# Kernel optimization log

Hardware: AMD Instinct MI355X
Metric: run time of the kernel (lower is better)

Reference implementation:

```python
import jax, jax.numpy as jnp
import numpy as np

N_NODES = 100000


def gcn_conv(x, W, b, src, dst, norm, n):
    # x: [N, Fin] -> [N, Fout]; PyG GCNConv: linear, then normalized scatter-add
    h = x @ W                                   # [N, Fout]
    msgs = h[src] * norm[:, None]               # gather + degree-normalize, [E2, Fout]
    out = jax.ops.segment_sum(msgs, dst, num_segments=n)  # scatter-add
    return out + b


def _norm_and_loops(edge_index, n):
    # add self-loops and compute symmetric normalization deg^-1/2 * deg^-1/2
    src = jnp.concatenate([edge_index[0], jnp.arange(n)])
    dst = jnp.concatenate([edge_index[1], jnp.arange(n)])
    deg = jax.ops.segment_sum(jnp.ones_like(dst, dtype=jnp.float32), dst, num_segments=n)
    dinv = jnp.where(deg > 0, jax.lax.rsqrt(jnp.maximum(deg, 1.0)), 0.0)
    norm = dinv[src] * dinv[dst]
    return src, dst, norm


def setup_inputs() -> dict:
    key = jax.random.key(0)
    ks = jax.random.split(key, 10)
    F_IN, H, C = 128, 128, 40
    x = jax.random.normal(ks[0], (N_NODES, F_IN), dtype=jnp.float32)
    edge_index = jax.random.randint(ks[1], (2, 3200000), 0, N_NODES, dtype=jnp.int64)
    def glorot(k, fan_in, fan_out):
        s = jnp.sqrt(6.0 / (fan_in + fan_out))
        return jax.random.uniform(k, (fan_in, fan_out), jnp.float32, -s, s)
    return {
        'x': x,
        'edge_index': edge_index,
        'W1': glorot(ks[2], F_IN, H), 'b1': jnp.zeros((H,), jnp.float32),
        'W2': glorot(ks[3], H, H),    'b2': jnp.zeros((H,), jnp.float32),
        'W3': glorot(ks[4], H, H),    'b3': jnp.zeros((H,), jnp.float32),
        'Wc': glorot(ks[5], H, C),    'bc': jnp.zeros((C,), jnp.float32),
    }


def reference(x, edge_index, W1, b1, W2, b2, W3, b3, Wc, bc):
    n = x.shape[0]
    src, dst, norm = _norm_and_loops(edge_index, n)
    h = jnp.tanh(gcn_conv(x, W1, b1, src, dst, norm, n))
    h = jnp.tanh(gcn_conv(h, W2, b2, src, dst, norm, n))
    h = jnp.tanh(gcn_conv(h, W3, b3, src, dst, norm, n))
    out = h @ Wc + bc
    return (out, h)
```

## Files before the change

### kernel.cpp

```cpp
#include <hip/hip_runtime.h>
#include <hip/hip_fp16.h>
#include <math.h>

#define H 128
#define BSTRIDE 5120
#define NPH 25


__global__ __launch_bounds__(256) void bin_kernel(const int* __restrict__ src,
        const int* __restrict__ dst, int* __restrict__ bucketFill,
        int* __restrict__ packed, int E, int nbk) {
    __shared__ int hcnt[1024];
    __shared__ int base[1024];
    __shared__ int cur[1024];
    int tid = threadIdx.x;
    for (int i = tid; i < nbk; i += 256) { hcnt[i] = 0; cur[i] = 0; }
    __syncthreads();
    int e0 = blockIdx.x * 8192;
    int e1 = min(e0 + 8192, E);
    for (int e = e0 + tid; e < e1; e += 256)
        atomicAdd(&hcnt[dst[e] >> 7], 1);
    __syncthreads();
    for (int i = tid; i < nbk; i += 256) {
        int c = hcnt[i];
        base[i] = c ? atomicAdd(&bucketFill[i], c) : 0;
    }
    __syncthreads();
    for (int e = e0 + tid; e < e1; e += 256) {
        int d = dst[e], s = src[e];
        int b = d >> 7;
        int r = atomicAdd(&cur[b], 1);
        packed[b * BSTRIDE + base[b] + r] = ((d & 127) << 17) | s;
    }
}

__global__ __launch_bounds__(256) void fine_kernel(const int* __restrict__ packed,
        const int* __restrict__ bucketFill,
        int* __restrict__ rowptr, int* __restrict__ col, float* __restrict__ dinv,
        int N, int E) {
    __shared__ int cnt[128 * NPH];
    __shared__ int cur[128 * NPH];
    __shared__ int lcnt[128], lofs[128];
    __shared__ int red[256];
    int b = blockIdx.x;
    int tid = threadIdx.x;
    int m = bucketFill[b]; if (m > BSTRIDE) m = BSTRIDE;
    int n0 = b << 7;

    int psum = 0;
    for (int i = tid; i < b; i += 256) psum += bucketFill[i];
    red[tid] = psum;
    for (int i = tid; i < 128 * NPH; i += 256) cnt[i] = 0;
    __syncthreads();
    #pragma unroll
    for (int off = 128; off > 0; off >>= 1) {
        if (tid < off) red[tid] += red[tid + off];
        __syncthreads();
    }
    int base = red[0];
    if (b == 0 && tid == 0) rowptr[N] = E;

    const int* pk = packed + (size_t)b * BSTRIDE;
    for (int i = tid; i < m; i += 256) {
        int p = pk[i];
        int ld = p >> 17, s = p & 131071;
        atomicAdd(&cnt[ld * NPH + (s >> 12)], 1);
    }
    __syncthreads();
    if (tid < 128) {
        int t = 0;
        #pragma unroll
        for (int q = 0; q < NPH; ++q) t += cnt[tid * NPH + q];
        lcnt[tid] = t;
    }
    __syncthreads();
    if (tid == 0) {
        int acc = 0;
        #pragma unroll 4
        for (int i = 0; i < 128; ++i) { lofs[i] = acc; acc += lcnt[i]; }
    }
    __syncthreads();
    if (tid < 128) {
        int o = lofs[tid];
        #pragma unroll
        for (int q = 0; q < NPH; ++q) {
            int c = cnt[tid * NPH + q];
            cur[tid * NPH + q] = o;
            o += c;
        }
        int node = n0 + tid;
        if (node < N) {
            rowptr[node] = base + lofs[tid];
            dinv[node] = rsqrtf((float)(lcnt[tid] + 1));
        }
    }
    __syncthreads();
    for (int i = tid; i < m; i += 256) {
        int p = pk[i];
        int ld = p >> 17, s = p & 131071;
        int r = atomicAdd(&cur[ld * NPH + (s >> 12)], 1);
        col[base + r] = s;
    }
}


__device__ inline unsigned pack2(float x, float y) {
    __half2 h = __floats2half2_rn(x, y);
    return *(unsigned*)&h;
}

__global__ __launch_bounds__(256) void gemm128_kernel(const float* __restrict__ A,
        const float* __restrict__ W, const float* __restrict__ scale,
        unsigned short* __restrict__ C, int N) {
    __shared__ float As[64][H + 1];
    int tid = threadIdx.x;
    int r0 = blockIdx.x * 64;

    #pragma unroll
    for (int i = 0; i < 8; ++i) {
        int lin = tid + i * 256;
        int r = lin >> 5;
        int c4 = (lin & 31) << 2;
        float4 v = make_float4(0.f, 0.f, 0.f, 0.f);
        if (r0 + r < N) v = *(const float4*)&A[(size_t)(r0 + r) * H + c4];
        As[r][c4 + 0] = v.x; As[r][c4 + 1] = v.y;
        As[r][c4 + 2] = v.z; As[r][c4 + 3] = v.w;
    }
    __syncthreads();

    int row = tid & 63;
    int c0 = __builtin_amdgcn_readfirstlane((tid >> 6) << 5);

    float acc[32];
    #pragma unroll
    for (int j = 0; j < 32; ++j) acc[j] = 0.f;

    for (int k = 0; k < H; ++k) {
        float a = As[row][k];
        #pragma unroll
        for (int j = 0; j < 32; ++j)
            acc[j] = fmaf(a, W[k * H + c0 + j], acc[j]);
    }

    int gr = r0 + row;
    if (gr < N) {
        float s = scale[gr];
        unsigned short* Crow = C + (size_t)gr * H;
        #pragma unroll
        for (int j = 0; j < 32; j += 8) {
            uint4 w;
            w.x = pack2(acc[j + 0] * s, acc[j + 1] * s);
            w.y = pack2(acc[j + 2] * s, acc[j + 3] * s);
            w.z = pack2(acc[j + 4] * s, acc[j + 5] * s);
            w.w = pack2(acc[j + 6] * s, acc[j + 7] * s);
            *(uint4*)&Crow[c0 + j] = w;
        }
    }
}


__device__ inline void add8(float* a, uint4 v) {
    float2 f;
    f = __half22float2(*(const __half2*)&v.x); a[0] += f.x; a[1] += f.y;
    f = __half22float2(*(const __half2*)&v.y); a[2] += f.x; a[3] += f.y;
    f = __half22float2(*(const __half2*)&v.z); a[4] += f.x; a[5] += f.y;
    f = __half22float2(*(const __half2*)&v.w); a[6] += f.x; a[7] += f.y;
}

__global__ __launch_bounds__(256) void spmm_kernel(const unsigned short* __restrict__ lin,
        const int* __restrict__ rowptr, const int* __restrict__ col,
        const float* __restrict__ dinv, const float* __restrict__ bias,
        float* __restrict__ out, int N) {
    int tid = threadIdx.x;
    int node = blockIdx.x * 16 + (tid >> 4);
    if (node >= N) return;
    int cq = tid & 15;

    int beg = rowptr[node];
    int end = rowptr[node + 1];

    const uint4* linv = (const uint4*)lin;

    float acc[8];
    {
        uint4 sv = linv[(size_t)node * 16 + cq];
        float2 f;
        f = __half22float2(*(const __half2*)&sv.x); acc[0] = f.x; acc[1] = f.y;
        f = __half22float2(*(const __half2*)&sv.y); acc[2] = f.x; acc[3] = f.y;
        f = __half22float2(*(const __half2*)&sv.z); acc[4] = f.x; acc[5] = f.y;
        f = __half22float2(*(const __half2*)&sv.w); acc[6] = f.x; acc[7] = f.y;
    }

    int e = beg;
    for (; e + 4 <= end; e += 4) {
        int s0 = col[e], s1 = col[e + 1], s2 = col[e + 2], s3 = col[e + 3];
        uint4 v0 = linv[(size_t)s0 * 16 + cq];
        uint4 v1 = linv[(size_t)s1 * 16 + cq];
        uint4 v2 = linv[(size_t)s2 * 16 + cq];
        uint4 v3 = linv[(size_t)s3 * 16 + cq];
        add8(acc, v0);
        add8(acc, v1);
        add8(acc, v2);
        add8(acc, v3);
    }
    for (; e < end; ++e) {
        uint4 v = linv[(size_t)col[e] * 16 + cq];
        add8(acc, v);
    }

    float d = dinv[node];
    int c8 = cq << 3;
    float4 r0, r1;
    r0.x = tanhf(fmaf(acc[0], d, bias[c8 + 0]));
    r0.y = tanhf(fmaf(acc[1], d, bias[c8 + 1]));
    r0.z = tanhf(fmaf(acc[2], d, bias[c8 + 2]));
    r0.w = tanhf(fmaf(acc[3], d, bias[c8 + 3]));
    r1.x = tanhf(fmaf(acc[4], d, bias[c8 + 4]));
    r1.y = tanhf(fmaf(acc[5], d, bias[c8 + 5]));
    r1.z = tanhf(fmaf(acc[6], d, bias[c8 + 6]));
    r1.w = tanhf(fmaf(acc[7], d, bias[c8 + 7]));
    float4* op = (float4*)out + (size_t)node * 32 + (cq << 1);
    op[0] = r0;
    op[1] = r1;
}


__global__ __launch_bounds__(256) void classifier_kernel(const float* __restrict__ h,
        const float* __restrict__ Wc, const float* __restrict__ bc,
        float* __restrict__ out, int N, int Cout) {
    __shared__ float As[64][H + 1];
    int tid = threadIdx.x;
    int r0 = blockIdx.x * 64;

    #pragma unroll
    for (int i = 0; i < 8; ++i) {
        int lin = tid + i * 256;
        int r = lin >> 5;
        int c4 = (lin & 31) << 2;
        float4 v = make_float4(0.f, 0.f, 0.f, 0.f);
        if (r0 + r < N) v = *(const float4*)&h[(size_t)(r0 + r) * H + c4];
        As[r][c4 + 0] = v.x; As[r][c4 + 1] = v.y;
        As[r][c4 + 2] = v.z; As[r][c4 + 3] = v.w;
    }
    __syncthreads();

    int row = tid & 63;
    int c0 = __builtin_amdgcn_readfirstlane((tid >> 6) * 10);

    float acc[10];
    #pragma unroll
    for (int j = 0; j < 10; ++j) acc[j] = bc[c0 + j];

    for (int k = 0; k < H; ++k) {
        float a = As[row][k];
        #pragma unroll
        for (int j = 0; j < 10; ++j)
            acc[j] = fmaf(a, Wc[k * Cout + c0 + j], acc[j]);
    }

    int gr = r0 + row;
    if (gr < N) {
        float* orow = out + (size_t)gr * Cout + c0;
        #pragma unroll
        for (int j = 0; j < 10; ++j) orow[j] = acc[j];
    }
}


extern "C" void kernel_launch(void* const* d_in, const int* in_sizes, int n_in,
                              void* d_out, int out_size, void* d_ws, size_t ws_size,
                              hipStream_t stream) {
    const float* x  = (const float*)d_in[0];
    const int* eidx = (const int*)d_in[1];
    const float* W1 = (const float*)d_in[2];
    const float* b1 = (const float*)d_in[3];
    const float* W2 = (const float*)d_in[4];
    const float* b2 = (const float*)d_in[5];
    const float* W3 = (const float*)d_in[6];
    const float* b3 = (const float*)d_in[7];
    const float* Wc = (const float*)d_in[8];
    const float* bc = (const float*)d_in[9];

    int N    = in_sizes[0] / H;
    int E    = in_sizes[1] / 2;
    int Cout = in_sizes[8] / H;
    int nbk  = (N + 127) >> 7;

    const int* srcp = eidx;
    const int* dstp = eidx + E;

    float* out  = (float*)d_out;
    float* hOut = out + (size_t)N * Cout;

    char* p = (char*)d_ws;
    float* hAf      = (float*)p;  p += (size_t)N * H * 4;
    int*   col      = (int*)p;    p += (size_t)E * 4;
    int*   rowptr   = (int*)p;    p += (size_t)(N + 1) * 4;
    float* dinv     = (float*)p;  p += (size_t)N * 4;
    int*   bFill    = (int*)p;    p += 1024 * 4;
    unsigned short* hA = (unsigned short*)hAf;
    int*   packed   = (int*)hAf;

    int gg = (N + 63) / 64;
    int gs = (N + 15) / 16;
    int gb = (E + 8191) / 8192;

    hipMemsetAsync(bFill, 0, (size_t)nbk * 4, stream);
    bin_kernel<<<gb, 256, 0, stream>>>(srcp, dstp, bFill, packed, E, nbk);
    fine_kernel<<<nbk, 256, 0, stream>>>(packed, bFill, rowptr, col, dinv, N, E);

    gemm128_kernel<<<gg, 256, 0, stream>>>(x, W1, dinv, hA, N);
    spmm_kernel<<<gs, 256, 0, stream>>>(hA, rowptr, col, dinv, b1, hOut, N);
    gemm128_kernel<<<gg, 256, 0, stream>>>(hOut, W2, dinv, hA, N);
    spmm_kernel<<<gs, 256, 0, stream>>>(hA, rowptr, col, dinv, b2, hOut, N);
    gemm128_kernel<<<gg, 256, 0, stream>>>(hOut, W3, dinv, hA, N);
    spmm_kernel<<<gs, 256, 0, stream>>>(hA, rowptr, col, dinv, b3, hOut, N);
    classifier_kernel<<<gg, 256, 0, stream>>>(hOut, Wc, bc, out, N, Cout);
}
```

Before: 803.7 us.

## Use fp16 MFMA matrix cores for the dense 128x128 GEMM

Replaces the scalar FP32 FMA loop in the per-layer linear transform with MFMA 16x16x32 fp16 instructions. Inputs and the transposed weight are converted to fp16 and staged in padded shared memory. Each wave computes a 64x32 output tile. This removes the ALU-bound inner loop but lowers input precision to fp16, and the output stores become scattered 2-byte writes instead of 16-byte vector stores.

```diff
diff --git a/kernel.cpp b/kernel.cpp
--- a/kernel.cpp
+++ b/kernel.cpp
@@ -5,6 +5,9 @@
 #define H 128
 #define BSTRIDE 5120
 #define NPH 25
+
+typedef _Float16 f16x8 __attribute__((ext_vector_type(8)));
+typedef float f32x4 __attribute__((ext_vector_type(4)));
 
 
 __global__ __launch_bounds__(256) void bin_kernel(const int* __restrict__ src,
@@ -104,15 +107,11 @@
 }
 
 
-__device__ inline unsigned pack2(float x, float y) {
-    __half2 h = __floats2half2_rn(x, y);
-    return *(unsigned*)&h;
-}
-
 __global__ __launch_bounds__(256) void gemm128_kernel(const float* __restrict__ A,
         const float* __restrict__ W, const float* __restrict__ scale,
         unsigned short* __restrict__ C, int N) {
-    __shared__ float As[64][H + 1];
+    __shared__ _Float16 Ah[64][H + 8];
+    __shared__ _Float16 Wt[H][H + 8];
     int tid = threadIdx.x;
     int r0 = blockIdx.x * 64;
 
@@ -123,37 +122,63 @@
         int c4 = (lin & 31) << 2;
         float4 v = make_float4(0.f, 0.f, 0.f, 0.f);
         if (r0 + r < N) v = *(const float4*)&A[(size_t)(r0 + r) * H + c4];
-        As[r][c4 + 0] = v.x; As[r][c4 + 1] = v.y;
-        As[r][c4 + 2] = v.z; As[r][c4 + 3] = v.w;
-    }
-    __syncthreads();
-
-    int row = tid & 63;
-    int c0 = __builtin_amdgcn_readfirstlane((tid >> 6) << 5);
-
-    float acc[32];
-    #pragma unroll
-    for (int j = 0; j < 32; ++j) acc[j] = 0.f;
-
-    for (int k = 0; k < H; ++k) {
-        float a = As[row][k];
-        #pragma unroll
-        for (int j = 0; j < 32; ++j)
-            acc[j] = fmaf(a, W[k * H + c0 + j], acc[j]);
-    }
-
-    int gr = r0 + row;
-    if (gr < N) {
-        float s = scale[gr];
-        unsigned short* Crow = C + (size_t)gr * H;
-        #pragma unroll
-        for (int j = 0; j < 32; j += 8) {
-            uint4 w;
-            w.x = pack2(acc[j + 0] * s, acc[j + 1] * s);
-            w.y = pack2(acc[j + 2] * s, acc[j + 3] * s);
-            w.z = pack2(acc[j + 4] * s, acc[j + 5] * s);
-            w.w = pack2(acc[j + 6] * s, acc[j + 7] * s);
-            *(uint4*)&Crow[c0 + j] = w;
+        _Float16* ap = &Ah[r][c4];
+        ap[0] = (_Float16)v.x; ap[1] = (_Float16)v.y;
+        ap[2] = (_Float16)v.z; ap[3] = (_Float16)v.w;
+    }
+    #pragma unroll
+    for (int i = 0; i < 64; ++i) {
+        int lin = i * 256 + tid;
+        int k = lin >> 7, n = lin & 127;
+        Wt[n][k] = (_Float16)W[lin];
+    }
+    __syncthreads();
+
+    int wid = tid >> 6;
+    int lane = tid & 63;
+    int cb = wid << 5;
+    int m16 = lane & 15;
+    int kg = lane >> 4;
+
+    f32x4 acc[4][2];
+    #pragma unroll
+    for (int rt = 0; rt < 4; ++rt)
+        #pragma unroll
+        for (int ct = 0; ct < 2; ++ct)
+            acc[rt][ct] = (f32x4){0.f, 0.f, 0.f, 0.f};
+
+    #pragma unroll
+    for (int kc = 0; kc < 4; ++kc) {
+        int kbase = kc * 32 + kg * 8;
+        f16x8 afr[4], bfr[2];
+        #pragma unroll
+        for (int rt = 0; rt < 4; ++rt)
+            afr[rt] = *(const f16x8*)&Ah[rt * 16 + m16][kbase];
+        #pragma unroll
+        for (int ct = 0; ct < 2; ++ct)
+            bfr[ct] = *(const f16x8*)&Wt[cb + ct * 16 + m16][kbase];
+        #pragma unroll
+        for (int rt = 0; rt < 4; ++rt)
+            #pragma unroll
+            for (int ct = 0; ct < 2; ++ct)
+                acc[rt][ct] = __builtin_amdgcn_mfma_f32_16x16x32_f16(
+                        afr[rt], bfr[ct], acc[rt][ct], 0, 0, 0);
+    }
+
+    #pragma unroll
+    for (int rt = 0; rt < 4; ++rt) {
+        int rowb = r0 + rt * 16 + (lane >> 4) * 4;
+        #pragma unroll
+        for (int reg = 0; reg < 4; ++reg) {
+            int grow = rowb + reg;
+            if (grow < N) {
+                float s = scale[grow];
+                unsigned short* Crow = C + (size_t)grow * H + cb + (lane & 15);
+                __half h0 = __float2half_rn(acc[rt][0][reg] * s);
+                __half h1 = __float2half_rn(acc[rt][1][reg] * s);
+                Crow[0]  = *(unsigned short*)&h0;
+                Crow[16] = *(unsigned short*)&h1;
+            }
         }
     }
 }
```

After: 705.3 us. 12.2% less time.
